# Kernel optimization log

Measured on AMD Instinct MI355X. Metric: run time of the kernel, lower is better.

The kernel has to match this reference:

```python
import jax, jax.numpy as jnp
import numpy as np

HIDDEN = 512
HEADS = 8
HEAD_DIM = HIDDEN // HEADS
MAX_DIST = 10
B, N = 16, 512
EPS = 1e-5


def _layer_norm(x, g, b):
    mu = jnp.mean(x, axis=-1, keepdims=True)
    var = jnp.mean(jnp.square(x - mu), axis=-1, keepdims=True)
    return (x - mu) * jax.lax.rsqrt(var + EPS) * g + b


def setup_inputs() -> dict:
    key = jax.random.key(0)
    ks = jax.random.split(key, 16)
    s = 0.02
    inp = {
        "x": jax.random.normal(ks[0], (B, N, HIDDEN), jnp.float32),
        "distances": jax.random.randint(ks[1], (B, N, N), 0, MAX_DIST, jnp.int32),
        "edge_features": jax.random.normal(ks[2], (B, N, N), jnp.float32),
        "attn_mask": jax.random.randint(ks[3], (B, N), 0, 2).astype(bool),
        "Wq": jax.random.normal(ks[4], (HIDDEN, HIDDEN), jnp.float32) * s,
        "bq": jnp.zeros((HIDDEN,), jnp.float32),
        "Wk": jax.random.normal(ks[5], (HIDDEN, HIDDEN), jnp.float32) * s,
        "bk": jnp.zeros((HIDDEN,), jnp.float32),
        "Wv": jax.random.normal(ks[6], (HIDDEN, HIDDEN), jnp.float32) * s,
        "bv": jnp.zeros((HIDDEN,), jnp.float32),
        "Wo": jax.random.normal(ks[7], (HIDDEN, HIDDEN), jnp.float32) * s,
        "bo": jnp.zeros((HIDDEN,), jnp.float32),
        "spatial_emb": jax.random.normal(ks[8], (MAX_DIST, HEADS), jnp.float32) * s,
        "edge_w": jax.random.normal(ks[9], (HEADS,), jnp.float32) * s,
        "edge_b": jnp.zeros((HEADS,), jnp.float32),
        "ln1_g": jnp.ones((HIDDEN,), jnp.float32),
        "ln1_b": jnp.zeros((HIDDEN,), jnp.float32),
        "ln2_g": jnp.ones((HIDDEN,), jnp.float32),
        "ln2_b": jnp.zeros((HIDDEN,), jnp.float32),
        "W1": jax.random.normal(ks[10], (HIDDEN, 4 * HIDDEN), jnp.float32) * s,
        "b1": jnp.zeros((4 * HIDDEN,), jnp.float32),
        "W2": jax.random.normal(ks[11], (4 * HIDDEN, HIDDEN), jnp.float32) * s,
        "b2": jnp.zeros((HIDDEN,), jnp.float32),
    }
    return inp


def reference(x, distances, edge_features, attn_mask, Wq, bq, Wk, bk, Wv, bv,
              Wo, bo, spatial_emb, edge_w, edge_b, ln1_g, ln1_b, ln2_g, ln2_b,
              W1, b1, W2, b2):
    b, n, _ = x.shape
    q = (x @ Wq + bq).reshape(b, n, HEADS, HEAD_DIM)
    k = (x @ Wk + bk).reshape(b, n, HEADS, HEAD_DIM)
    v = (x @ Wv + bv).reshape(b, n, HEADS, HEAD_DIM)
    # [b, h, i, j] attention scores
    scores = jnp.einsum('bihd,bjhd->bhij', q, k) / np.sqrt(HEAD_DIM).astype(np.float32)
    spatial_bias = spatial_emb[distances]                       # [b, i, j, h]
    edge_bias = edge_features[..., None] * edge_w + edge_b      # [b, i, j, h]
    scores = scores + jnp.transpose(spatial_bias + edge_bias, (0, 3, 1, 2))
    scores = jnp.where(attn_mask[:, None, None, :], -jnp.inf, scores)
    attn = jax.nn.softmax(scores, axis=-1)
    out = jnp.einsum('bhij,bjhd->bihd', attn, v).reshape(b, n, HIDDEN)
    out = out @ Wo + bo
    h = _layer_norm(x + out, ln1_g, ln1_b)
    ffn = jax.nn.relu(h @ W1 + b1) @ W2 + b2
    return _layer_norm(h + ffn, ln2_g, ln2_b)
```

## Files before the change

kernel.cpp:

```cpp
#include <hip/hip_runtime.h>
#include <stdint.h>
#include <stddef.h>

#define SEQ   512
#define HID   512
#define NHEAD 8
#define HD    64
#define NBATCH 16
#define NTOK  8192
#define MAXD  10

typedef __attribute__((ext_vector_type(8))) short short8;
typedef __attribute__((ext_vector_type(4))) float f32x4;

typedef __attribute__((address_space(3))) void        as3_void;
typedef const __attribute__((address_space(1))) void  as1_cvoid;

#define MFMA16(a,b,c) __builtin_amdgcn_mfma_f32_16x16x32_bf16((a),(b),(c),0,0,0)

__device__ __forceinline__ float bf2f(uint16_t u){ return __uint_as_float(((uint32_t)u)<<16); }
__device__ __forceinline__ uint16_t f2bf(float f){
  uint32_t i = __float_as_uint(f);
  return (uint16_t)((i + 0x7fffu + ((i>>16)&1u)) >> 16);
}

enum { EPI_BF16=0, EPI_F32=3, EPI_RELU=4 };

__global__ __launch_bounds__(256) void f2bf_kernel(
    const float* __restrict__ in, uint16_t* __restrict__ out, int n4)
{
  int i = blockIdx.x*256 + threadIdx.x;
  if (i < n4){
    float4 v = *(const float4*)(in + (size_t)i*4);
    *(ushort4*)(out + (size_t)i*4) =
        make_ushort4(f2bf(v.x), f2bf(v.y), f2bf(v.z), f2bf(v.w));
  }
}

__global__ __launch_bounds__(256) void transpose_all(
    const float* __restrict__ Wq, const float* __restrict__ Wk,
    const float* __restrict__ Wv, const float* __restrict__ Wo,
    const float* __restrict__ W1, const float* __restrict__ W2,
    uint16_t* __restrict__ tq, uint16_t* __restrict__ tk,
    uint16_t* __restrict__ tv, uint16_t* __restrict__ to_,
    uint16_t* __restrict__ t1, uint16_t* __restrict__ t2)
{
  __shared__ uint16_t tile[32][33];
  int id = blockIdx.x;
  const float* in; uint16_t* out; int R, C, tx, ty;
  if (id < 1024) {
    int m = id >> 8, loc = id & 255;
    in  = (m==0)?Wq:(m==1)?Wk:(m==2)?Wv:Wo;
    out = (m==0)?tq:(m==1)?tk:(m==2)?tv:to_;
    R = 512; C = 512; ty = loc>>4; tx = loc&15;
  } else if (id < 2048) {
    int loc = id-1024; in=W1; out=t1; R=512; C=2048; ty=loc>>6; tx=loc&63;
  } else {
    int loc = id-2048; in=W2; out=t2; R=2048; C=512; ty=loc>>4; tx=loc&15;
  }
  int bx = tx*32, by = ty*32;
  int lx = threadIdx.x & 31, ly = threadIdx.x >> 5;
  #pragma unroll
  for (int i=ly; i<32; i+=8) tile[i][lx] = f2bf(in[(size_t)(by+i)*C + bx+lx]);
  __syncthreads();
  #pragma unroll
  for (int i=ly; i<32; i+=8) out[(size_t)(bx+i)*R + by+lx] = tile[lx][i];
}

__global__ __launch_bounds__(512) void pack_bias(
    const int*   __restrict__ dist,
    const float* __restrict__ edge,
    const int*   __restrict__ mask,
    uint32_t*    __restrict__ outp)
{
  __shared__ int   dl[16][260];
  __shared__ float el[16][260];
  __shared__ int   ml[512];
  const int b  = blockIdx.y;
  const int it = blockIdx.x;
  const int t  = threadIdx.x;
  ml[t] = mask[b*SEQ + t];

  #pragma unroll
  for (int jh=0; jh<2; ++jh){
    if (jh) __syncthreads();
    {
      const int r  = t >> 5;
      const int c0 = (t & 31) * 8;
      const size_t g = ((size_t)b*SEQ + it*16 + r)*SEQ + jh*256 + c0;
      *(int4*)&dl[r][c0]     = *(const int4*)&dist[g];
      *(int4*)&dl[r][c0+4]   = *(const int4*)&dist[g+4];
      *(float4*)&el[r][c0]   = *(const float4*)&edge[g];
      *(float4*)&el[r][c0+4] = *(const float4*)&edge[g+4];
    }
    __syncthreads();
    {
      const int i   = t & 15;
      const int j0p = (t >> 4) * 8;
      const int jt  = jh*4 + (j0p >> 6);
      const int jn  = (j0p >> 4) & 3;
      const int lg  = (j0p & 15) >> 2;
      uint32_t w[8];
      #pragma unroll
      for (int e=0; e<8; ++e){
        const int jl = j0p + e;
        const int jg = jh*256 + jl;
        const uint32_t d  = (uint32_t)dl[i][jl] & 0xFFu;
        const uint32_t mk = (ml[jg] ? 1u : 0u) << 8;
        w[e] = ((uint32_t)f2bf(el[i][jl]) << 16) | mk | d;
      }
      uint32_t* ob = outp + ((((size_t)b*32 + it)*8 + jt)*64)*16;
      const int lane0 = lg*16 + i, lane1 = (lg+1)*16 + i;
      *(uint4*)&ob[lane0*16 + jn*4] = make_uint4(w[0],w[1],w[2],w[3]);
      *(uint4*)&ob[lane1*16 + jn*4] = make_uint4(w[4],w[5],w[6],w[7]);
    }
  }
}

template<int BM>
__device__ __forceinline__ void gemm_tile_mainloop(
    const uint16_t* __restrict__ A, const uint16_t* __restrict__ Bt,
    int K, int m0, int n0, uint16_t* lA, uint16_t* lB,
    f32x4 acc[4][(BM==128)?4:2])
{
  constexpr int NJ  = (BM==128)?4:2;
  constexpr int ARD = BM/32;
  const int t = threadIdx.x;
  const int w = t>>6, l = t&63;
  const int lg = l>>4, lc = l&15;
  const int wr = (BM==128)?(w>>1):0;
  const int wc = (BM==128)?(w&1):w;
  const int kSteps = K>>6;
  for (int kt=0; kt<kSteps; ++kt){
    const int k0 = kt<<6;
    #pragma unroll
    for (int rd=0; rd<ARD; ++rd){
      const int e   = rd*2048 + t*8;
      const int row = e>>6, col = e&63;
      const uint16_t* ga = A + (size_t)(m0+row)*K + (k0+col);
      char* la = (char*)lA + rd*4096 + w*1024;
      __builtin_amdgcn_global_load_lds((as1_cvoid*)ga, (as3_void*)la, 16, 0, 0);
    }
    #pragma unroll
    for (int rd=0; rd<4; ++rd){
      const int e   = rd*2048 + t*8;
      const int row = e>>6, col = e&63;
      const uint16_t* gb = Bt + (size_t)(n0+row)*K + (k0+col);
      char* lb = (char*)lB + rd*4096 + w*1024;
      __builtin_amdgcn_global_load_lds((as1_cvoid*)gb, (as3_void*)lb, 16, 0, 0);
    }
    __syncthreads();
    #pragma unroll
    for (int kk=0; kk<2; ++kk){
      short8 af[4], bfr[NJ];
      #pragma unroll
      for (int i=0;i<4;i++)
        af[i]  = *(const short8*)&lA[(wr*64 + i*16 + lc)*64 + kk*32 + lg*8];
      #pragma unroll
      for (int j=0;j<NJ;j++)
        bfr[j] = *(const short8*)&lB[(wc*16*NJ + j*16 + lc)*64 + kk*32 + lg*8];
      #pragma unroll
      for (int i=0;i<4;i++)
        #pragma unroll
        for (int j=0;j<NJ;j++)
          acc[i][j] = MFMA16(af[i], bfr[j], acc[i][j]);
    }
    __syncthreads();
  }
}

template<int EPI, int BM>
__global__ __launch_bounds__(256,2) void gemm_bt(
    const uint16_t* __restrict__ A, const uint16_t* __restrict__ Bt,
    const float* __restrict__ bias, void* __restrict__ outp,
    int M, int N, int K)
{
  constexpr int NJ = (BM==128)?4:2;
  __shared__ uint16_t lA[BM*64];
  __shared__ uint16_t lB[128*64];
  f32x4 acc[4][NJ];
  #pragma unroll
  for (int i=0;i<4;i++)
    #pragma unroll
    for (int j=0;j<NJ;j++){ f32x4 z = {0.f,0.f,0.f,0.f}; acc[i][j]=z; }
  const int m0 = blockIdx.y*BM, n0 = blockIdx.x*128;
  gemm_tile_mainloop<BM>(A, Bt, K, m0, n0, lA, lB, acc);

  const int t=threadIdx.x, w=t>>6, l=t&63, lg=l>>4, lc=l&15;
  const int wr=(BM==128)?(w>>1):0, wc=(BM==128)?(w&1):w;
  #pragma unroll
  for (int j=0;j<NJ;j++){
    const int col = n0 + wc*16*NJ + j*16 + lc;
    const float bs = bias[col];
    #pragma unroll
    for (int i=0;i<4;i++){
      const int rowb = m0 + wr*64 + i*16 + lg*4;
      #pragma unroll
      for (int r=0;r<4;r++){
        float v = acc[i][j][r] + bs;
        if constexpr (EPI==EPI_RELU)   v = fmaxf(v, 0.f);
        if constexpr (EPI==EPI_F32)
          ((float*)outp)[(size_t)(rowb+r)*N + col] = v;
        else
          ((uint16_t*)outp)[(size_t)(rowb+r)*N + col] = f2bf(v);
      }
    }
  }
}

__global__ __launch_bounds__(256,2) void qkv_gemm(
    const uint16_t* __restrict__ x,
    const uint16_t* __restrict__ wtq, const uint16_t* __restrict__ wtk,
    const uint16_t* __restrict__ wtv,
    const float* __restrict__ bq, const float* __restrict__ bk,
    const float* __restrict__ bv,
    uint16_t* __restrict__ qo, uint16_t* __restrict__ kp,
    uint16_t* __restrict__ vp)
{
  __shared__ uint16_t lA[128*64];
  __shared__ uint16_t lB[128*64];
  const int z = blockIdx.z;
  const uint16_t* Bt = (z==0)?wtq:(z==1)?wtk:wtv;
  const float*  bias = (z==0)?bq :(z==1)?bk :bv;
  f32x4 acc[4][4];
  #pragma unroll
  for (int i=0;i<4;i++)
    #pragma unroll
    for (int j=0;j<4;j++){ f32x4 zz = {0.f,0.f,0.f,0.f}; acc[i][j]=zz; }
  const int m0 = blockIdx.y*128, n0 = blockIdx.x*128;
  gemm_tile_mainloop<128>(x, Bt, HID, m0, n0, lA, lB, acc);

  const int t=threadIdx.x, w=t>>6, l=t&63, lg=l>>4, lc=l&15, wr=w>>1, wc=w&1;
  if (z==0){
    const float scale = 0.125f;
    #pragma unroll
    for (int j=0;j<4;j++){
      const int col = n0 + wc*64 + j*16 + lc;
      const float bs = bias[col];
      #pragma unroll
      for (int i=0;i<4;i++){
        const int rowb = m0 + wr*64 + i*16 + lg*4;
        #pragma unroll
        for (int r=0;r<4;r++)
          qo[(size_t)(rowb+r)*HID + col] = f2bf((acc[i][j][r] + bs)*scale);
      }
    }
  } else if (z==1){
    #pragma unroll
    for (int j=0;j<4;j++){
      const int col = n0 + wc*64 + j*16 + lc;
      const float bs = bias[col];
      const int h_ = col>>6, cm = col&63, kk = cm>>5, lgk = (cm>>3)&3, e = col&7;
      #pragma unroll
      for (int i=0;i<4;i++){
        const int rowb = m0 + wr*64 + i*16 + lg*4;
        #pragma unroll
        for (int r=0;r<4;r++){
          const int tok = rowb + r;
          const int b_ = tok>>9, tl = tok&511;
          const int jt = tl>>6, jn = (tl>>4)&3, lck = tl&15;
          kp[((((size_t)(b_*8+h_)*8 + jt)*4 + jn)*2 + kk)*512
             + (lgk*16 + lck)*8 + e] = f2bf(acc[i][j][r] + bs);
        }
      }
    }
  } else {
    #pragma unroll
    for (int j=0;j<4;j++){
      const int col = n0 + wc*64 + j*16 + lc;
      const float bs = bias[col];
      const int h_ = col>>6, dn = (col>>4)&3, lcv = col&15;
      #pragma unroll
      for (int i=0;i<4;i++){
        const int rowb = m0 + wr*64 + i*16 + lg*4;
        const int b_ = rowb>>9, tl = rowb&511;
        const int jt = tl>>6, kk = (tl>>5)&1, lgv = (tl>>3)&3, e0 = tl&7;
        *(ushort4*)&vp[((((size_t)(b_*8+h_)*8 + jt)*2 + kk)*4 + dn)*512
                       + (lgv*16 + lcv)*8 + e0] =
            make_ushort4(f2bf(acc[i][j][0]+bs), f2bf(acc[i][j][1]+bs),
                         f2bf(acc[i][j][2]+bs), f2bf(acc[i][j][3]+bs));
      }
    }
  }
}

__global__ __launch_bounds__(512,4) void attn_kernel(
    const uint16_t* __restrict__ q,
    const uint16_t* __restrict__ kp,
    const uint16_t* __restrict__ vp,
    const uint32_t* __restrict__ biasp,
    const float*    __restrict__ semb,
    const float*    __restrict__ ew,
    const float*    __restrict__ eb,
    uint16_t* __restrict__ out)
{
  __shared__ float sp_rep[NHEAD][32][11];
  __shared__ uint16_t plds[NHEAD][2][16*64];
  const int b  = blockIdx.y;
  const int it = blockIdx.x;
  const int i0 = it*16;
  const int t  = threadIdx.x;
  const int h  = t>>6, l = t&63, lg = l>>4, lc = l&15;
  for (int i = t; i < NHEAD*32*MAXD; i += 512){
    const int hh = i / (32*MAXD), rem = i % (32*MAXD);
    const int a = rem / MAXD, d = rem % MAXD;
    sp_rep[hh][a][d] = semb[d*NHEAD + hh];
  }
  __syncthreads();
  const float ewf = ew[h], ebf = eb[h];
  const float* spl = &sp_rep[h][l&31][0];
  char* pbase = (char*)&plds[h][0][0];
  const int swz = (lc&7)<<4;

  short8 qf[2];
  #pragma unroll
  for (int kk=0;kk<2;kk++)
    qf[kk] = *(const short8*)&q[(size_t)(b*SEQ + i0 + lc)*HID + h*HD + kk*32 + lg*8];

  const uint4* bp = (const uint4*)(biasp + (((size_t)b*32 + it)*8)*64*16);
  const uint16_t* kpb = kp + (size_t)(b*8+h)*8*4*2*512 + l*8;
  const uint16_t* vpb = vp + (size_t)(b*8+h)*8*2*4*512 + l*8;

  float mrun[2] = {-1e30f, -1e30f};
  float lrun[2] = {0.f, 0.f};
  f32x4 oacc[2][4];
  #pragma unroll
  for (int s=0;s<2;s++)
    #pragma unroll
    for (int dn=0;dn<4;dn++){ f32x4 z={0.f,0.f,0.f,0.f}; oacc[s][dn]=z; }

  #pragma unroll
  for (int p=0; p<4; ++p){
    #pragma unroll
    for (int s=0; s<2; ++s){
      const int jt = s*4 + p;
      uint32_t uw[16];
      {
        const uint4* bq_ = bp + (jt*64 + l)*4;
        *(uint4*)&uw[0]  = bq_[0];
        *(uint4*)&uw[4]  = bq_[1];
        *(uint4*)&uw[8]  = bq_[2];
        *(uint4*)&uw[12] = bq_[3];
      }
      f32x4 st[4];
      #pragma unroll
      for (int jn=0;jn<4;jn++){ f32x4 z={0.f,0.f,0.f,0.f}; st[jn]=z; }
      __builtin_amdgcn_s_setprio(1);
      #pragma unroll
      for (int jn=0;jn<4;jn++){
        #pragma unroll
        for (int kk=0;kk<2;kk++){
          short8 kf = *(const short8*)&kpb[(size_t)((jt*4 + jn)*2 + kk)*512];
          st[jn] = MFMA16(kf, qf[kk], st[jn]);
        }
      }
      __builtin_amdgcn_s_setprio(0);
      float tmax = -1e30f;
      #pragma unroll
      for (int jn=0;jn<4;jn++){
        #pragma unroll
        for (int r=0;r<4;r++){
          const uint32_t u = uw[jn*4+r];
          float sv = st[jn][r] + spl[u & 0xFFu]
                   + bf2f((uint16_t)(u >> 16))*ewf + ebf;
          if (u & 0x100u) sv = -1e30f;
          st[jn][r] = sv;
          tmax = fmaxf(tmax, sv);
        }
      }
      {
        float tm = fmaxf(tmax, __shfl_xor(tmax, 16, 64));
        tm = fmaxf(tm, __shfl_xor(tm, 32, 64));
        float mnew = fmaxf(mrun[s], tm);
        mnew = fmaxf(mnew, -1e20f);
        const float c = __expf(mrun[s] - mnew);
        mrun[s] = mnew;
        float lsum = 0.f;
        char* pb = pbase + s*(16*64*2) + lc*128;
        #pragma unroll
        for (int jn=0;jn<4;jn++){
          float p0 = __expf(st[jn][0]-mnew);
          float p1 = __expf(st[jn][1]-mnew);
          float p2 = __expf(st[jn][2]-mnew);
          float p3 = __expf(st[jn][3]-mnew);
          lsum += (p0+p1)+(p2+p3);
          *(ushort4*)(pb + (((jn*16 + lg*4)*2) ^ swz)) =
              make_ushort4(f2bf(p0), f2bf(p1), f2bf(p2), f2bf(p3));
        }
        lrun[s] = lrun[s]*c + lsum;
        #pragma unroll
        for (int r=0;r<4;r++){
          const float cr = __shfl(c, lg*4+r, 64);
          #pragma unroll
          for (int dn=0;dn<4;dn++) oacc[s][dn][r] *= cr;
        }
      }
    }
    #pragma unroll
    for (int s=0; s<2; ++s){
      const int jt = s*4 + p;
      char* pb = pbase + s*(16*64*2) + lc*128;
      __builtin_amdgcn_s_setprio(1);
      #pragma unroll
      for (int kk=0;kk<2;kk++){
        short8 pa = *(const short8*)(pb + (((kk*32 + lg*8)*2) ^ swz));
        #pragma unroll
        for (int dn=0;dn<4;dn++){
          short8 vb = *(const short8*)&vpb[(size_t)((jt*2 + kk)*4 + dn)*512];
          oacc[s][dn] = MFMA16(pa, vb, oacc[s][dn]);
        }
      }
      __builtin_amdgcn_s_setprio(0);
    }
  }
  {
    const float mm = fmaxf(mrun[0], mrun[1]);
    const float c0 = __expf(mrun[0]-mm), c1 = __expf(mrun[1]-mm);
    float ls = lrun[0]*c0 + lrun[1]*c1;
    ls += __shfl_xor(ls, 16, 64);
    ls += __shfl_xor(ls, 32, 64);
    const float inv = 1.f/ls;
    #pragma unroll
    for (int r=0;r<4;r++){
      const float cr0 = __shfl(c0, lg*4+r, 64);
      const float cr1 = __shfl(c1, lg*4+r, 64);
      const float ir  = __shfl(inv, lg*4+r, 64);
      const size_t orow = ((size_t)b*SEQ + i0 + lg*4 + r)*HID;
      #pragma unroll
      for (int dn=0;dn<4;dn++)
        out[orow + h*HD + dn*16 + lc] =
            f2bf((oacc[0][dn][r]*cr0 + oacc[1][dn][r]*cr1)*ir);
    }
  }
}

__global__ __launch_bounds__(256) void ln_kernel(
    const float* __restrict__ a, const float* __restrict__ bsrc,
    const float* __restrict__ g, const float* __restrict__ bb,
    float* __restrict__ of, uint16_t* __restrict__ ob)
{
  const int row = blockIdx.x*4 + (threadIdx.x>>6);
  const int l = threadIdx.x & 63;
  const float* ar = a    + (size_t)row*HID;
  const float* br = bsrc + (size_t)row*HID;
  float u[8];
  {
    float4 a0 = *(const float4*)(ar + l*4);
    float4 a1 = *(const float4*)(ar + 256 + l*4);
    float4 b0 = *(const float4*)(br + l*4);
    float4 b1 = *(const float4*)(br + 256 + l*4);
    u[0]=a0.x+b0.x; u[1]=a0.y+b0.y; u[2]=a0.z+b0.z; u[3]=a0.w+b0.w;
    u[4]=a1.x+b1.x; u[5]=a1.y+b1.y; u[6]=a1.z+b1.z; u[7]=a1.w+b1.w;
  }
  float s=0.f, ss=0.f;
  #pragma unroll
  for (int e=0;e<8;e++){ s += u[e]; ss += u[e]*u[e]; }
  #pragma unroll
  for (int off=32; off>=1; off>>=1){
    s  += __shfl_xor(s,  off, 64);
    ss += __shfl_xor(ss, off, 64);
  }
  const float mu  = s*(1.f/512.f);
  const float inv = rsqrtf(ss*(1.f/512.f) - mu*mu + 1e-5f);
  float y[8];
  #pragma unroll
  for (int e=0;e<4;e++){
    int c0 = l*4+e, c1 = 256+l*4+e;
    y[e]   = (u[e]  -mu)*inv*g[c0] + bb[c0];
    y[4+e] = (u[4+e]-mu)*inv*g[c1] + bb[c1];
  }
  if (of){
    float* orow = of + (size_t)row*HID;
    *(float4*)(orow + l*4)       = make_float4(y[0],y[1],y[2],y[3]);
    *(float4*)(orow + 256 + l*4) = make_float4(y[4],y[5],y[6],y[7]);
  }
  if (ob){
    uint16_t* brow = ob + (size_t)row*HID;
    *(ushort4*)(brow + l*4)       = make_ushort4(f2bf(y[0]),f2bf(y[1]),f2bf(y[2]),f2bf(y[3]));
    *(ushort4*)(brow + 256 + l*4) = make_ushort4(f2bf(y[4]),f2bf(y[5]),f2bf(y[6]),f2bf(y[7]));
  }
}

extern "C" void kernel_launch(void* const* d_in, const int* in_sizes, int n_in,
                              void* d_out, int out_size, void* d_ws, size_t ws_size,
                              hipStream_t stream)
{
  (void)in_sizes; (void)n_in; (void)out_size; (void)ws_size;
  const float* x    = (const float*)d_in[0];
  const int*   dist = (const int*)  d_in[1];
  const float* edge = (const float*)d_in[2];
  const int*   mask = (const int*)  d_in[3];
  const float* Wq = (const float*)d_in[4];
  const float* bq = (const float*)d_in[5];
  const float* Wk = (const float*)d_in[6];
  const float* bk = (const float*)d_in[7];
  const float* Wv = (const float*)d_in[8];
  const float* bv = (const float*)d_in[9];
  const float* Wo = (const float*)d_in[10];
  const float* bo = (const float*)d_in[11];
  const float* semb = (const float*)d_in[12];
  const float* ew   = (const float*)d_in[13];
  const float* eb   = (const float*)d_in[14];
  const float* ln1g = (const float*)d_in[15];
  const float* ln1b = (const float*)d_in[16];
  const float* ln2g = (const float*)d_in[17];
  const float* ln2b = (const float*)d_in[18];
  const float* W1 = (const float*)d_in[19];
  const float* b1 = (const float*)d_in[20];
  const float* W2 = (const float*)d_in[21];
  const float* b2 = (const float*)d_in[22];

  char* ws = (char*)d_ws;
  uint16_t* xb16  = (uint16_t*)ws;
  uint16_t* qbuf  = xb16  + (size_t)NTOK*HID;
  uint16_t* kpbuf = qbuf  + (size_t)NTOK*HID;
  uint16_t* vpbuf = kpbuf + (size_t)NTOK*HID;
  uint16_t* aobuf = vpbuf + (size_t)NTOK*HID;
  uint16_t* f1buf = qbuf;
  uint32_t* biasp = (uint32_t*)(ws + (size_t)5*NTOK*HID*2);
  float*    tbuf  = (float*)biasp;
  float*    t2buf = tbuf;
  float*    hbuf  = tbuf + (size_t)NTOK*HID;
  uint16_t* hb16  = (uint16_t*)(hbuf + (size_t)NTOK*HID);
  uint16_t* wt    = hb16 + (size_t)NTOK*HID;
  uint16_t* wtq = wt;
  uint16_t* wtk = wtq + 512*512;
  uint16_t* wtv = wtk + 512*512;
  uint16_t* wto = wtv + 512*512;
  uint16_t* wt1 = wto + 512*512;
  uint16_t* wt2 = wt1 + 512*2048;

  pack_bias<<<dim3(32,16), 512, 0, stream>>>(dist, edge, mask, biasp);

  transpose_all<<<3072, 256, 0, stream>>>(Wq,Wk,Wv,Wo,W1,W2, wtq,wtk,wtv,wto,wt1,wt2);

  f2bf_kernel<<<4096, 256, 0, stream>>>(x, xb16, NTOK*HID/4);

  qkv_gemm<<<dim3(4,64,3), 256, 0, stream>>>(xb16, wtq,wtk,wtv, bq,bk,bv,
                                             qbuf, kpbuf, vpbuf);

  attn_kernel<<<dim3(32,16), 512, 0, stream>>>(qbuf, kpbuf, vpbuf, biasp,
                                               semb, ew, eb, aobuf);

  gemm_bt<EPI_F32,64><<<dim3(4,128), 256, 0, stream>>>(aobuf, wto, bo, tbuf, NTOK, HID, HID);

  ln_kernel<<<2048, 256, 0, stream>>>(tbuf, x, ln1g, ln1b, hbuf, hb16);

  gemm_bt<EPI_RELU,128><<<dim3(16,64), 256, 0, stream>>>(hb16, wt1, b1, f1buf, NTOK, 2048, HID);

  gemm_bt<EPI_F32,64><<<dim3(4,128), 256, 0, stream>>>(f1buf, wt2, b2, t2buf, NTOK, HID, 2048);

  ln_kernel<<<2048, 256, 0, stream>>>(t2buf, hbuf, ln2g, ln2b, (float*)d_out, nullptr);
}
```

Baseline: 178.6 us.

## Swizzle GEMM LDS layout, add 64-wide N tiles, and swap grid axes

Adds an XOR swizzle on the 16-byte column chunks that are written to LDS and read back as MFMA fragments, aiming to remove LDS bank conflicts. Adds a BN template parameter so the N=512 GEMMs (output projection and FFN2) use 64x64 tiles, doubling their block count to fill more CUs. Also swaps the grid axes so consecutive blocks walk along M and share the same weight tile. The smaller tiles lower arithmetic intensity per block, and the 64x64 config leaves each wave with only 4 MFMA accumulators.

```diff
diff --git a/kernel.cpp b/kernel.cpp
--- a/kernel.cpp
+++ b/kernel.cpp
@@ -117,34 +117,38 @@
   }
 }
 
-template<int BM>
+template<int BM, int BN>
 __device__ __forceinline__ void gemm_tile_mainloop(
     const uint16_t* __restrict__ A, const uint16_t* __restrict__ Bt,
     int K, int m0, int n0, uint16_t* lA, uint16_t* lB,
-    f32x4 acc[4][(BM==128)?4:2])
-{
-  constexpr int NJ  = (BM==128)?4:2;
+    f32x4 acc[4][(BM==128)?4:((BN==128)?2:1)])
+{
+  constexpr int NJ  = (BM==128)?4:((BN==128)?2:1);
   constexpr int ARD = BM/32;
+  constexpr int BRD = BN/32;
   const int t = threadIdx.x;
   const int w = t>>6, l = t&63;
   const int lg = l>>4, lc = l&15;
   const int wr = (BM==128)?(w>>1):0;
   const int wc = (BM==128)?(w&1):w;
+  const int swz = lc & 7;
   const int kSteps = K>>6;
   for (int kt=0; kt<kSteps; ++kt){
     const int k0 = kt<<6;
     #pragma unroll
     for (int rd=0; rd<ARD; ++rd){
       const int e   = rd*2048 + t*8;
-      const int row = e>>6, col = e&63;
+      const int row = e>>6;
+      const int col = (((e>>3)&7) ^ (row&7))*8;
       const uint16_t* ga = A + (size_t)(m0+row)*K + (k0+col);
       char* la = (char*)lA + rd*4096 + w*1024;
       __builtin_amdgcn_global_load_lds((as1_cvoid*)ga, (as3_void*)la, 16, 0, 0);
     }
     #pragma unroll
-    for (int rd=0; rd<4; ++rd){
+    for (int rd=0; rd<BRD; ++rd){
       const int e   = rd*2048 + t*8;
-      const int row = e>>6, col = e&63;
+      const int row = e>>6;
+      const int col = (((e>>3)&7) ^ (row&7))*8;
       const uint16_t* gb = Bt + (size_t)(n0+row)*K + (k0+col);
       char* lb = (char*)lB + rd*4096 + w*1024;
       __builtin_amdgcn_global_load_lds((as1_cvoid*)gb, (as3_void*)lb, 16, 0, 0);
@@ -152,13 +156,14 @@
     __syncthreads();
     #pragma unroll
     for (int kk=0; kk<2; ++kk){
+      const int cc = (kk*4 + lg) ^ swz;
       short8 af[4], bfr[NJ];
       #pragma unroll
       for (int i=0;i<4;i++)
-        af[i]  = *(const short8*)&lA[(wr*64 + i*16 + lc)*64 + kk*32 + lg*8];
+        af[i]  = *(const short8*)&lA[(wr*64 + i*16 + lc)*64 + cc*8];
       #pragma unroll
       for (int j=0;j<NJ;j++)
-        bfr[j] = *(const short8*)&lB[(wc*16*NJ + j*16 + lc)*64 + kk*32 + lg*8];
+        bfr[j] = *(const short8*)&lB[(wc*16*NJ + j*16 + lc)*64 + cc*8];
       #pragma unroll
       for (int i=0;i<4;i++)
         #pragma unroll
@@ -169,22 +174,22 @@
   }
 }
 
-template<int EPI, int BM>
+template<int EPI, int BM, int BN>
 __global__ __launch_bounds__(256,2) void gemm_bt(
     const uint16_t* __restrict__ A, const uint16_t* __restrict__ Bt,
     const float* __restrict__ bias, void* __restrict__ outp,
     int M, int N, int K)
 {
-  constexpr int NJ = (BM==128)?4:2;
+  constexpr int NJ = (BM==128)?4:((BN==128)?2:1);
   __shared__ uint16_t lA[BM*64];
-  __shared__ uint16_t lB[128*64];
+  __shared__ uint16_t lB[BN*64];
   f32x4 acc[4][NJ];
   #pragma unroll
   for (int i=0;i<4;i++)
     #pragma unroll
     for (int j=0;j<NJ;j++){ f32x4 z = {0.f,0.f,0.f,0.f}; acc[i][j]=z; }
-  const int m0 = blockIdx.y*BM, n0 = blockIdx.x*128;
-  gemm_tile_mainloop<BM>(A, Bt, K, m0, n0, lA, lB, acc);
+  const int m0 = blockIdx.x*BM, n0 = blockIdx.y*BN;
+  gemm_tile_mainloop<BM,BN>(A, Bt, K, m0, n0, lA, lB, acc);
 
   const int t=threadIdx.x, w=t>>6, l=t&63, lg=l>>4, lc=l&15;
   const int wr=(BM==128)?(w>>1):0, wc=(BM==128)?(w&1):w;
@@ -227,8 +232,8 @@
   for (int i=0;i<4;i++)
     #pragma unroll
     for (int j=0;j<4;j++){ f32x4 zz = {0.f,0.f,0.f,0.f}; acc[i][j]=zz; }
-  const int m0 = blockIdx.y*128, n0 = blockIdx.x*128;
-  gemm_tile_mainloop<128>(x, Bt, HID, m0, n0, lA, lB, acc);
+  const int m0 = blockIdx.x*128, n0 = blockIdx.y*128;
+  gemm_tile_mainloop<128,128>(x, Bt, HID, m0, n0, lA, lB, acc);
 
   const int t=threadIdx.x, w=t>>6, l=t&63, lg=l>>4, lc=l&15, wr=w>>1, wc=w&1;
   if (z==0){
@@ -536,19 +541,19 @@
 
   f2bf_kernel<<<4096, 256, 0, stream>>>(x, xb16, NTOK*HID/4);
 
-  qkv_gemm<<<dim3(4,64,3), 256, 0, stream>>>(xb16, wtq,wtk,wtv, bq,bk,bv,
+  qkv_gemm<<<dim3(64,4,3), 256, 0, stream>>>(xb16, wtq,wtk,wtv, bq,bk,bv,
                                              qbuf, kpbuf, vpbuf);
 
   attn_kernel<<<dim3(32,16), 512, 0, stream>>>(qbuf, kpbuf, vpbuf, biasp,
                                                semb, ew, eb, aobuf);
 
-  gemm_bt<EPI_F32,64><<<dim3(4,128), 256, 0, stream>>>(aobuf, wto, bo, tbuf, NTOK, HID, HID);
+  gemm_bt<EPI_F32,64,64><<<dim3(128,8), 256, 0, stream>>>(aobuf, wto, bo, tbuf, NTOK, HID, HID);
 
   ln_kernel<<<2048, 256, 0, stream>>>(tbuf, x, ln1g, ln1b, hbuf, hb16);
 
-  gemm_bt<EPI_RELU,128><<<dim3(16,64), 256, 0, stream>>>(hb16, wt1, b1, f1buf, NTOK, 2048, HID);
-
-  gemm_bt<EPI_F32,64><<<dim3(4,128), 256, 0, stream>>>(f1buf, wt2, b2, t2buf, NTOK, HID, 2048);
+  gemm_bt<EPI_RELU,128,128><<<dim3(64,16), 256, 0, stream>>>(hb16, wt1, b1, f1buf, NTOK, 2048, HID);
+
+  gemm_bt<EPI_F32,64,64><<<dim3(128,8), 256, 0, stream>>>(f1buf, wt2, b2, t2buf, NTOK, HID, 2048);
 
   ln_kernel<<<2048, 256, 0, stream>>>(t2buf, hbuf, ln2g, ln2b, (float*)d_out, nullptr);
 }
```

Measured after the change: 163.2 us. 1.09x faster.
